# Kernel tuning notes

Hardware: AMD Instinct MI355X
Metric: run time of the kernel (lower is better)

The kernel has to match this reference:

```python
import jax, jax.numpy as jnp
import numpy as np

jax.config.update("jax_enable_x64", True)

P = 2013265921          # NTT-friendly prime 15 * 2**27 + 1 (int64-safe proxy for BLS12-377 Fr)
GEN = 31                # generator of the multiplicative group of F_P
LOGN = 22
N = 1 << LOGN           # domain_size
C = 4                   # columns, as in the module docstring example


def _pow_table(base, n):
    """powers[k] = base**k mod P for k in [0, n), built by repeated doubling (vectorized)."""
    pw = np.ones(n, dtype=np.int64)
    cur = base % P
    step = 1
    while step < n:
        hi = min(2 * step, n)
        pw[step:hi] = (pw[:hi - step] * cur) % P
        cur = (cur * cur) % P
        step *= 2
    return pw


def setup_inputs() -> dict:
    key = jax.random.key(0)
    x = jax.random.randint(key, (N, C), 0, P, dtype=jnp.int64)
    omega = pow(GEN, (P - 1) // N, P)          # primitive N-th root of unity
    omega_inv = pow(omega, P - 2, P)           # its inverse (Fermat)
    twiddles = jnp.asarray(_pow_table(omega_inv, N // 2))  # omega_inv**k, k < N/2  (the 'Params' table)
    n_inv = jnp.asarray(pow(N, P - 2, P), dtype=jnp.int64)  # N^{-1} mod P
    return {"input": x, "twiddles": twiddles, "n_inv": n_inv}


def reference(input, twiddles, n_inv):
    """Inverse NTT over F_P, columns transformed independently. Output in natural order."""
    n, c = input.shape
    logn = n.bit_length() - 1
    # bit-reversal permutation indices (static; computed with numpy)
    idx = np.arange(n)
    rev = np.zeros(n, dtype=np.int64)
    for i in range(logn):
        rev = (rev << 1) | ((idx >> i) & 1)
    x = input[rev]
    # iterative Cooley-Tukey butterflies, logn stages
    for s in range(1, logn + 1):
        m = 1 << s
        half = m >> 1
        w = twiddles[:: n // m]                 # [half] = omega_inv**(j * n/m)
        xr = x.reshape(-1, m, c)                # [n/m, m, c]
        lo, hi = xr[:, :half], xr[:, half:]
        t = (w[None, :, None] * hi) % P         # modular twiddle multiply
        x = jnp.concatenate([(lo + t) % P, (lo - t) % P], axis=1).reshape(n, c)
    return (x * n_inv) % P                      # scale by N^{-1}
```

## Files before the change

kernel.cpp:

```cpp
#include <hip/hip_runtime.h>
#include <stdint.h>

static constexpr uint32_t P = 2013265921u;
static constexpr int      LOGM = 11;
static constexpr int      MSZ  = 1 << LOGM;
static constexpr int      NCOL = 4;

__host__ __device__ constexpr uint32_t neg_pinv32() {
    uint32_t x = 1u;
    for (int i = 0; i < 5; ++i) x *= 2u - P * x;
    return 0u - x;
}
static constexpr uint32_t NEG_PINV = neg_pinv32();
static constexpr uint32_t R1 = (uint32_t)(((uint64_t)1 << 32) % P);
static constexpr uint32_t R2 = (uint32_t)(((uint64_t)R1 * R1) % P);

__device__ __forceinline__ uint32_t mont_mul(uint32_t a, uint32_t b) {
    uint32_t tlo = a * b;
    uint32_t thi = __umulhi(a, b);
    uint32_t m   = tlo * NEG_PINV;
    uint32_t r   = thi + __umulhi(m, P) + (tlo != 0u);
    uint32_t s   = r - P;
    return s < r ? s : r;
}
__device__ __forceinline__ uint32_t to_mont(uint32_t a) { return mont_mul(a, R2); }

__device__ __forceinline__ uint32_t shoup_mul(uint32_t w, uint32_t wp, uint32_t x) {
    uint32_t q = __umulhi(wp, x);
    uint32_t t = w * x - q * P;
    uint32_t s = t - P;
    return s < t ? s : t;
}
__device__ __forceinline__ uint32_t add_p(uint32_t a, uint32_t b) {
    uint32_t r = a + b, s = r - P; return s < r ? s : r;
}
__device__ __forceinline__ uint32_t sub_p(uint32_t a, uint32_t b) {
    uint32_t r = a - b, s = r + P; return s < r ? s : r;
}
__device__ __forceinline__ uint4 mm4(uint32_t w, uint4 v) {
    return make_uint4(mont_mul(w, v.x), mont_mul(w, v.y),
                      mont_mul(w, v.z), mont_mul(w, v.w));
}
__device__ __forceinline__ void bf4_sh(uint4& L, uint4& H, uint2 w) {
    uint4 t = make_uint4(shoup_mul(w.x, w.y, H.x), shoup_mul(w.x, w.y, H.y),
                         shoup_mul(w.x, w.y, H.z), shoup_mul(w.x, w.y, H.w));
    uint4 l = L;
    L = make_uint4(add_p(l.x, t.x), add_p(l.y, t.y), add_p(l.z, t.z), add_p(l.w, t.w));
    H = make_uint4(sub_p(l.x, t.x), sub_p(l.y, t.y), sub_p(l.z, t.z), sub_p(l.w, t.w));
}
__device__ __forceinline__ void bf4_mont(uint4& L, uint4& H, uint32_t wm) {
    uint4 t = mm4(wm, H);
    uint4 l = L;
    L = make_uint4(add_p(l.x, t.x), add_p(l.y, t.y), add_p(l.z, t.z), add_p(l.w, t.w));
    H = make_uint4(sub_p(l.x, t.x), sub_p(l.y, t.y), sub_p(l.z, t.z), sub_p(l.w, t.w));
}
__device__ __forceinline__ void bf4_triv(uint4& L, uint4& H) {
    uint4 l = L, h = H;
    L = make_uint4(add_p(l.x, h.x), add_p(l.y, h.y), add_p(l.z, h.z), add_p(l.w, h.w));
    H = make_uint4(sub_p(l.x, h.x), sub_p(l.y, h.y), sub_p(l.z, h.z), sub_p(l.w, h.w));
}

__device__ __forceinline__ int g_sw(int el) {
    return el ^ (((el >> 3) ^ (el >> 6)) & 7);
}
__device__ __forceinline__ int fidx(int el, int c4) { return (g_sw(el) << 2) | c4; }

__device__ __forceinline__ void radix8_sh(uint4 x[8],
        uint2 ta, uint2 tb0, uint2 tb1,
        uint2 tc0, uint2 tc1, uint2 tc2, uint2 tc3) {
    bf4_sh(x[0], x[1], ta);  bf4_sh(x[2], x[3], ta);
    bf4_sh(x[4], x[5], ta);  bf4_sh(x[6], x[7], ta);
    bf4_sh(x[0], x[2], tb0); bf4_sh(x[1], x[3], tb1);
    bf4_sh(x[4], x[6], tb0); bf4_sh(x[5], x[7], tb1);
    bf4_sh(x[0], x[4], tc0); bf4_sh(x[1], x[5], tc1);
    bf4_sh(x[2], x[6], tc2); bf4_sh(x[3], x[7], tc3);
}

template <bool PASS2>
__global__ __launch_bounds__(1024, 2) void intt_pass(
        const uint4* __restrict__ src, uint4* __restrict__ dst,
        const uint32_t* __restrict__ tw,
        const uint32_t* __restrict__ ninv_p)
{
    __shared__ uint4 buf[MSZ * NCOL];
    __shared__ uint2 stab[2048];

    const int      t   = threadIdx.x;
    const int      c4  = t & 3;
    const int      sub = t >> 2;
    const uint32_t bid = blockIdx.x;
    const uint32_t grp = ((bid & 7u) << 6) | (bid >> 3);
    const uint32_t c   = (grp << 2) | (uint32_t)c4;

    uint32_t wv[2]; int ev[2];
#pragma unroll
    for (int q = 0; q < 2; ++q) {
        int e = t + (q << 10);
        ev[q] = e;
        if (e < 2047) {
            uint32_t ep1 = (uint32_t)e + 1u;
            int sm1 = 31 - __clz((int)ep1);
            uint32_t j = ep1 - (1u << sm1);
            wv[q] = tw[j << (21 - sm1)];
        }
    }

    const uint32_t r8 = __brev((uint32_t)sub) >> 24;
    uint4 x[8];
#pragma unroll
    for (int m = 0; m < 8; ++m) {
        uint32_t r3 = __brev((uint32_t)m) >> 29;
        x[m] = src[((r3 << 8) | r8) * (uint32_t)MSZ + c];
    }

#pragma unroll
    for (int q = 0; q < 2; ++q) {
        if (ev[q] < 2047) {
            uint32_t w  = wv[q];
            uint32_t wp = (uint32_t)((((uint64_t)w) << 32) / P);
            stab[ev[q]] = make_uint2(w, wp);
        }
    }

    const uint32_t u1 = to_mont(tw[1u << 20]);
    const uint32_t u2 = to_mont(tw[1u << 19]);
    const uint32_t u3 = to_mont(tw[3u << 19]);

    bf4_triv(x[0], x[1]);  bf4_triv(x[2], x[3]);
    bf4_triv(x[4], x[5]);  bf4_triv(x[6], x[7]);
    bf4_triv(x[0], x[2]);  bf4_mont(x[1], x[3], u1);
    bf4_triv(x[4], x[6]);  bf4_mont(x[5], x[7], u1);
    bf4_triv(x[0], x[4]);  bf4_mont(x[1], x[5], u2);
    bf4_mont(x[2], x[6], u1); bf4_mont(x[3], x[7], u3);
#pragma unroll
    for (int m = 0; m < 8; ++m) buf[fidx(8 * sub + m, c4)] = x[m];
    __syncthreads();

    {
        const int L = sub & 7, hi = sub >> 3;
        const int base = (hi << 6) | L;
#pragma unroll
        for (int m = 0; m < 8; ++m) x[m] = buf[fidx(base | (m << 3), c4)];
        radix8_sh(x, stab[7 + L], stab[15 + L], stab[23 + L],
                     stab[31 + L], stab[39 + L], stab[47 + L], stab[55 + L]);
#pragma unroll
        for (int m = 0; m < 8; ++m) buf[fidx(base | (m << 3), c4)] = x[m];
    }
    __syncthreads();

    {
        const int L = sub & 63, hi = sub >> 6;
        const int base = (hi << 9) | L;
#pragma unroll
        for (int m = 0; m < 8; ++m) x[m] = buf[fidx(base | (m << 6), c4)];
        radix8_sh(x, stab[63 + L], stab[127 + L], stab[191 + L],
                     stab[255 + L], stab[319 + L], stab[383 + L], stab[447 + L]);
#pragma unroll
        for (int m = 0; m < 8; ++m) buf[fidx(base | (m << 6), c4)] = x[m];
    }
    __syncthreads();

    uint32_t nm = 0u, s256 = 0u, step512 = 0u, tm0 = 0u;
    if (PASS2) {
        nm = to_mont(*ninv_p);
    } else {
        s256    = to_mont(tw[c << 8]);
        step512 = mont_mul(s256, s256);
        tm0     = to_mont(tw[c * (uint32_t)sub]);
    }
#pragma unroll
    for (int gg = 0; gg < 2; ++gg) {
        const int lo = sub + (gg << 8);
        uint4 y[4];
#pragma unroll
        for (int m = 0; m < 4; ++m) y[m] = buf[fidx(lo | (m << 9), c4)];
        const uint2 t10  = stab[511 + lo];
        const uint2 t110 = stab[1023 + lo];
        const uint2 t111 = stab[1535 + lo];
        bf4_sh(y[0], y[1], t10);  bf4_sh(y[2], y[3], t10);
        bf4_sh(y[0], y[2], t110); bf4_sh(y[1], y[3], t111);

        if (!PASS2) {
            uint32_t tm = tm0;
#pragma unroll
            for (int m = 0; m < 4; ++m) {
                dst[c * (uint32_t)MSZ + (uint32_t)((m << 9) | lo)] = mm4(tm, y[m]);
                tm = mont_mul(tm, step512);
            }
            tm0 = mont_mul(tm0, s256);
        } else {
#pragma unroll
            for (int m = 0; m < 4; ++m)
                dst[(uint32_t)((m << 9) | lo) * (uint32_t)MSZ + c] = mm4(nm, y[m]);
        }
    }
}

extern "C" void kernel_launch(void* const* d_in, const int* in_sizes, int n_in,
                              void* d_out, int out_size, void* d_ws, size_t ws_size,
                              hipStream_t stream)
{
    const uint4*    x    = (const uint4*)d_in[0];
    const uint32_t* tw   = (const uint32_t*)d_in[1];
    const uint32_t* ninv = (const uint32_t*)d_in[2];
    uint4*          out  = (uint4*)d_out;

    intt_pass<false><<<dim3(512), dim3(1024), 0, stream>>>(x, out, tw, ninv);
    intt_pass<true ><<<dim3(512), dim3(1024), 0, stream>>>(out, out, tw, ninv);
}
```

Before: 201.9 us.

## Shrink blocks to one sub-FFT each and derive last-stage twiddles from a small table

Each block now handles a single 2048-point sub-transform with 256 threads instead of four sub-transforms with 1024 threads, which cuts shared memory per block from about 144KB to about 38KB. This allows more resident blocks and finer-grained scheduling. The 2048-entry Shoup twiddle table is replaced by a 511-entry Shoup table plus a 512-entry Montgomery table. The last two stages' twiddles are computed on the fly with Montgomery multiplies (squaring and a multiply by u1), trading shared-memory table setup and capacity for extra ALU work. The global access pattern changes too, since groups of four adjacent column rows are no longer loaded together per block.

```diff
diff --git a/kernel.cpp b/kernel.cpp
--- a/kernel.cpp
+++ b/kernel.cpp
@@ -4,7 +4,6 @@
 static constexpr uint32_t P = 2013265921u;
 static constexpr int      LOGM = 11;
 static constexpr int      MSZ  = 1 << LOGM;
-static constexpr int      NCOL = 4;
 
 __host__ __device__ constexpr uint32_t neg_pinv32() {
     uint32_t x = 1u;
@@ -63,7 +62,6 @@
 __device__ __forceinline__ int g_sw(int el) {
     return el ^ (((el >> 3) ^ (el >> 6)) & 7);
 }
-__device__ __forceinline__ int fidx(int el, int c4) { return (g_sw(el) << 2) | c4; }
 
 __device__ __forceinline__ void radix8_sh(uint4 x[8],
         uint2 ta, uint2 tb0, uint2 tb1,
@@ -77,33 +75,34 @@
 }
 
 template <bool PASS2>
-__global__ __launch_bounds__(1024, 2) void intt_pass(
+__global__ __launch_bounds__(256, 4) void intt_pass(
         const uint4* __restrict__ src, uint4* __restrict__ dst,
         const uint32_t* __restrict__ tw,
         const uint32_t* __restrict__ ninv_p)
 {
-    __shared__ uint4 buf[MSZ * NCOL];
-    __shared__ uint2 stab[2048];
+    __shared__ uint4    buf[MSZ];
+    __shared__ uint2    stab[511];
+    __shared__ uint32_t mtab[512];
 
     const int      t   = threadIdx.x;
-    const int      c4  = t & 3;
-    const int      sub = t >> 2;
+    const int      sub = t;
     const uint32_t bid = blockIdx.x;
-    const uint32_t grp = ((bid & 7u) << 6) | (bid >> 3);
-    const uint32_t c   = (grp << 2) | (uint32_t)c4;
+    const uint32_t c   = ((bid & 7u) << 8) | (bid >> 3);
 
     uint32_t wv[2]; int ev[2];
 #pragma unroll
     for (int q = 0; q < 2; ++q) {
-        int e = t + (q << 10);
+        int e = t + (q << 8);
         ev[q] = e;
-        if (e < 2047) {
+        if (e < 511) {
             uint32_t ep1 = (uint32_t)e + 1u;
             int sm1 = 31 - __clz((int)ep1);
             uint32_t j = ep1 - (1u << sm1);
             wv[q] = tw[j << (21 - sm1)];
         }
     }
+    uint32_t mv0 = tw[(uint32_t)t << 11];
+    uint32_t mv1 = tw[(uint32_t)(t + 256) << 11];
 
     const uint32_t r8 = __brev((uint32_t)sub) >> 24;
     uint4 x[8];
@@ -115,12 +114,14 @@
 
 #pragma unroll
     for (int q = 0; q < 2; ++q) {
-        if (ev[q] < 2047) {
+        if (ev[q] < 511) {
             uint32_t w  = wv[q];
             uint32_t wp = (uint32_t)((((uint64_t)w) << 32) / P);
             stab[ev[q]] = make_uint2(w, wp);
         }
     }
+    mtab[t]       = to_mont(mv0);
+    mtab[t + 256] = to_mont(mv1);
 
     const uint32_t u1 = to_mont(tw[1u << 20]);
     const uint32_t u2 = to_mont(tw[1u << 19]);
@@ -133,18 +134,18 @@
     bf4_triv(x[0], x[4]);  bf4_mont(x[1], x[5], u2);
     bf4_mont(x[2], x[6], u1); bf4_mont(x[3], x[7], u3);
 #pragma unroll
-    for (int m = 0; m < 8; ++m) buf[fidx(8 * sub + m, c4)] = x[m];
+    for (int m = 0; m < 8; ++m) buf[g_sw(8 * sub + m)] = x[m];
     __syncthreads();
 
     {
         const int L = sub & 7, hi = sub >> 3;
         const int base = (hi << 6) | L;
 #pragma unroll
-        for (int m = 0; m < 8; ++m) x[m] = buf[fidx(base | (m << 3), c4)];
+        for (int m = 0; m < 8; ++m) x[m] = buf[g_sw(base | (m << 3))];
         radix8_sh(x, stab[7 + L], stab[15 + L], stab[23 + L],
                      stab[31 + L], stab[39 + L], stab[47 + L], stab[55 + L]);
 #pragma unroll
-        for (int m = 0; m < 8; ++m) buf[fidx(base | (m << 3), c4)] = x[m];
+        for (int m = 0; m < 8; ++m) buf[g_sw(base | (m << 3))] = x[m];
     }
     __syncthreads();
 
@@ -152,11 +153,11 @@
         const int L = sub & 63, hi = sub >> 6;
         const int base = (hi << 9) | L;
 #pragma unroll
-        for (int m = 0; m < 8; ++m) x[m] = buf[fidx(base | (m << 6), c4)];
+        for (int m = 0; m < 8; ++m) x[m] = buf[g_sw(base | (m << 6))];
         radix8_sh(x, stab[63 + L], stab[127 + L], stab[191 + L],
                      stab[255 + L], stab[319 + L], stab[383 + L], stab[447 + L]);
 #pragma unroll
-        for (int m = 0; m < 8; ++m) buf[fidx(base | (m << 6), c4)] = x[m];
+        for (int m = 0; m < 8; ++m) buf[g_sw(base | (m << 6))] = x[m];
     }
     __syncthreads();
 
@@ -173,12 +174,12 @@
         const int lo = sub + (gg << 8);
         uint4 y[4];
 #pragma unroll
-        for (int m = 0; m < 4; ++m) y[m] = buf[fidx(lo | (m << 9), c4)];
-        const uint2 t10  = stab[511 + lo];
-        const uint2 t110 = stab[1023 + lo];
-        const uint2 t111 = stab[1535 + lo];
-        bf4_sh(y[0], y[1], t10);  bf4_sh(y[2], y[3], t10);
-        bf4_sh(y[0], y[2], t110); bf4_sh(y[1], y[3], t111);
+        for (int m = 0; m < 4; ++m) y[m] = buf[g_sw(lo | (m << 9))];
+        const uint32_t M    = mtab[lo];
+        const uint32_t t10  = mont_mul(M, M);
+        const uint32_t t111 = mont_mul(M, u1);
+        bf4_mont(y[0], y[1], t10);  bf4_mont(y[2], y[3], t10);
+        bf4_mont(y[0], y[2], M);    bf4_mont(y[1], y[3], t111);
 
         if (!PASS2) {
             uint32_t tm = tm0;
@@ -205,6 +206,6 @@
     const uint32_t* ninv = (const uint32_t*)d_in[2];
     uint4*          out  = (uint4*)d_out;
 
-    intt_pass<false><<<dim3(512), dim3(1024), 0, stream>>>(x, out, tw, ninv);
-    intt_pass<true ><<<dim3(512), dim3(1024), 0, stream>>>(out, out, tw, ninv);
-}
+    intt_pass<false><<<dim3(2048), dim3(256), 0, stream>>>(x, out, tw, ninv);
+    intt_pass<true ><<<dim3(2048), dim3(256), 0, stream>>>(out, out, tw, ninv);
+}
```

Result: slower. 212.9 us (+5.4%).
